# Optimization experiments

Hardware: AMD Instinct MI355X
Metric: run time of the kernel (lower is better)

Reference implementation:

```python
import jax, jax.numpy as jnp
import numpy as np

B = 1024
IN_SIZ = 16384
OUT_SIZ = 16384
C = 8          # channel_siz
NLVL = 10
IFS = IN_SIZ // 2 ** NLVL                                   # 16, in_filter_siz
KLVL = min(int(np.floor(np.log2(OUT_SIZ / 2))), NLVL)       # 10
OFS = OUT_SIZ // 2 ** KLVL                                  # 16, out_filter_siz
STD = 0.9


def setup_inputs() -> dict:
    key = jax.random.key(0)
    ks = jax.random.split(key, 2 * NLVL + 3)
    inp = {}
    inp["x"] = jax.random.normal(ks[0], (B, IN_SIZ, 1), jnp.float32)
    inp["in_filter"] = jax.random.normal(ks[1], (IFS, 1, C), jnp.float32) * STD
    inp["in_bias"] = jnp.zeros((C,), jnp.float32)
    for lvl in range(1, NLVL + 1):
        k = 2 ** lvl
        inp[f"W{lvl}"] = jax.random.normal(ks[2 * lvl], (k, 2, C, C), jnp.float32) * STD
        inp[f"b{lvl}"] = jnp.zeros((k, C), jnp.float32)
    inp["fea_dense"] = jax.random.normal(ks[-1], (2 ** KLVL, C, OFS), jnp.float32) * STD
    return inp


def _level(v, W, b):
    # v: [Kp, B, L, C] parent branches; W: [2*Kp, 2, C, C]; b: [2*Kp, C]
    # kernel-2 stride-2 conv1d: out[t] = relu(x[2t] @ W[0] + x[2t+1] @ W[1] + b)
    Kp, Bn, L, Cc = v.shape
    xp = v.reshape(Kp, Bn, L // 2, 2, Cc)
    xr = jnp.repeat(xp, 2, axis=0)  # child itk reads parent itk // 2
    y = jnp.einsum('kbtsc,kscd->kbtd', xr, W) + b[:, None, None, :]
    return jax.nn.relu(y)


def reference(x, in_filter, in_bias,
              W1, b1, W2, b2, W3, b3, W4, b4, W5, b5,
              W6, b6, W7, b7, W8, b8, W9, b9, W10, b10,
              fea_dense):
    Ws = [W1, W2, W3, W4, W5, W6, W7, W8, W9, W10]
    bs = [b1, b2, b3, b4, b5, b6, b7, b8, b9, b10]
    Bn = x.shape[0]
    # input conv1d: kernel=IFS, stride=IFS (non-overlapping) == blocked matmul
    xin = x[..., 0].reshape(Bn, 2 ** NLVL, IFS)                       # [B, 1024, 16]
    v = jax.nn.relu(jnp.einsum('bnf,fc->bnc', xin, in_filter[:, 0, :]) + in_bias)
    v = v[None]                                                        # [1, B, 1024, C]
    for lvl in range(NLVL):  # klvl == nlvl: all levels branch (tree doubling)
        v = _level(v, Ws[lvl], bs[lvl])
    # v: [2^klvl, B, 1, C] -> per-branch dense feature map
    out = jnp.einsum('kbc,kcf->bkf', v[:, :, 0, :], fea_dense)         # [B, 1024, OFS]
    return out.reshape(Bn, OUT_SIZ, 1)
```

## Files before the change

### kernel.cpp

```cpp
#include <hip/hip_runtime.h>

struct PrepPtrs { const float* W[7]; const float* Bv[7]; const float* F; const float* fb; };

__device__ __forceinline__ int scr(int ci) { return ci ^ ((ci >> 4) & 7); }
__device__ __forceinline__ int cz(int c) { return c ^ ((c >> 3) & 3); }

__device__ __forceinline__ float4 relu4(float4 a) {
  return make_float4(fmaxf(a.x,0.f), fmaxf(a.y,0.f), fmaxf(a.z,0.f), fmaxf(a.w,0.f));
}
__device__ __forceinline__ void fma4(float4& acc, float s, const float4& wv) {
  acc.x = fmaf(s, wv.x, acc.x); acc.y = fmaf(s, wv.y, acc.y);
  acc.z = fmaf(s, wv.z, acc.z); acc.w = fmaf(s, wv.w, acc.w);
}

__global__ void bfly_prep(PrepPtrs P, float* __restrict__ wt) {
  int e = blockIdx.x * 256 + threadIdx.x;
  if (e >= 510 * 68) return;
  int ent = e / 68, r = e % 68, dd = r & 3;
  float v; int dst;
  if (ent < 62) {
    dst = ent * 80 + r;
    if (ent < 60) {
      int lvl, base;
      if (ent < 4)       { lvl = 1; base = 0;  }
      else if (ent < 12) { lvl = 2; base = 4;  }
      else if (ent < 28) { lvl = 3; base = 12; }
      else               { lvl = 4; base = 28; }
      int k = (ent - base) >> 1, th = ent & 1;
      if (r < 64) { int s = r >> 5, c = (r >> 2) & 7;
        v = P.W[lvl-1][k*128 + s*64 + c*8 + th*4 + dd]; }
      else v = P.Bv[lvl-1][k*8 + th*4 + dd];
    } else {
      int th = ent - 60;
      if (r < 64) { int f = r >> 2; v = P.F[f*8 + th*4 + dd]; }
      else v = P.fb[th*4 + dd];
    }
  } else {
    int eb = ent - 62;
    int q = eb / 56, rem = eb % 56;
    int lvl, Kl, base;
    if (rem < 8)       { lvl = 5; Kl = 4;  base = 0;  }
    else if (rem < 24) { lvl = 6; Kl = 8;  base = 8;  }
    else               { lvl = 7; Kl = 16; base = 24; }
    int rr = rem - base, lk = rr >> 1, th = rr & 1;
    int kg = q * Kl + lk;
    if (r < 64) { int s = r >> 5, c = (r >> 2) & 7;
      v = P.W[lvl-1][kg*128 + s*64 + c*8 + th*4 + dd]; }
    else v = P.Bv[lvl-1][kg*8 + th*4 + dd];
    dst = 4960 + eb * 80 + r;
  }
  wt[dst] = v;
}

template<int L>
__device__ __forceinline__ void ka_level(const float4* __restrict__ src,
                                         float4* __restrict__ dst,
                                         const float4* __restrict__ wt4,
                                         int lane, int wq, int th) {
  constexpr int Kc = 1 << L, Tc = 1024 >> L;
  constexpr int entBase = (Kc - 2) * 2;
  constexpr int kIters = (L <= 2) ? 1 : (1 << (L - 2));
  constexpr int tIters = 4 / kIters;
#pragma unroll
  for (int ik = 0; ik < kIters; ++ik) {
    int k;
    if constexpr (L == 1) k = wq & 1;
    else if constexpr (L == 2) k = wq;
    else k = wq + 4 * ik;
    const float4* e4 = wt4 + (entBase + k * 2 + th) * 20;
    const int kp = k >> 1;
#pragma unroll
    for (int it = 0; it < tIters; ++it) {
      int t;
      if constexpr (L == 1) t = lane + (wq >> 1) * 64 + it * 128;
      else if constexpr (L == 2) t = lane + it * 64;
      else if constexpr (L == 3) t = lane + it * 64;
      else t = lane;
      int pb = kp * (2 * Tc) + 2 * t;
      float4 A0 = src[cz(pb)],        C0 = src[cz(pb + 1)];
      float4 A1 = src[cz(pb + 1024)], C1 = src[cz(pb + 1025)];
      float4 a = e4[16];
      fma4(a, A0.x, e4[0]);  fma4(a, A0.y, e4[1]);  fma4(a, A0.z, e4[2]);  fma4(a, A0.w, e4[3]);
      fma4(a, A1.x, e4[4]);  fma4(a, A1.y, e4[5]);  fma4(a, A1.z, e4[6]);  fma4(a, A1.w, e4[7]);
      fma4(a, C0.x, e4[8]);  fma4(a, C0.y, e4[9]);  fma4(a, C0.z, e4[10]); fma4(a, C0.w, e4[11]);
      fma4(a, C1.x, e4[12]); fma4(a, C1.y, e4[13]); fma4(a, C1.z, e4[14]); fma4(a, C1.w, e4[15]);
      dst[cz(th * 1024 + k * Tc + t)] = relu4(a);
    }
  }
}

__global__ __launch_bounds__(512, 2) void bfly_ka(
    const float* __restrict__ x, const float* __restrict__ wt,
    float* __restrict__ st1)
{
  __shared__ float4 sA[2048], sB[2048];
  const int tid = threadIdx.x, b = blockIdx.x;
  const int lane = tid & 63;
  const int wv = __builtin_amdgcn_readfirstlane(tid >> 6);
  const int th = wv & 1, wq = wv >> 1;
  const float4* wt4 = (const float4*)wt;

  {
    const float4* e4 = wt4 + (60 + th) * 20;
    const float* xb = x + (size_t)b * 16384;
#pragma unroll
    for (int i = 0; i < 4; ++i) {
      int n = lane + wq * 64 + i * 256;
      const float4* xr = (const float4*)(xb + n * 16);
      float4 x0 = xr[0], x1 = xr[1], x2 = xr[2], x3 = xr[3];
      float4 a = e4[16];
      fma4(a, x0.x, e4[0]);  fma4(a, x0.y, e4[1]);  fma4(a, x0.z, e4[2]);  fma4(a, x0.w, e4[3]);
      fma4(a, x1.x, e4[4]);  fma4(a, x1.y, e4[5]);  fma4(a, x1.z, e4[6]);  fma4(a, x1.w, e4[7]);
      fma4(a, x2.x, e4[8]);  fma4(a, x2.y, e4[9]);  fma4(a, x2.z, e4[10]); fma4(a, x2.w, e4[11]);
      fma4(a, x3.x, e4[12]); fma4(a, x3.y, e4[13]); fma4(a, x3.z, e4[14]); fma4(a, x3.w, e4[15]);
      sA[cz(th * 1024 + n)] = relu4(a);
    }
  }
  __syncthreads();
  ka_level<1>(sA, sB, wt4, lane, wq, th); __syncthreads();
  ka_level<2>(sB, sA, wt4, lane, wq, th); __syncthreads();
  ka_level<3>(sA, sB, wt4, lane, wq, th); __syncthreads();
  ka_level<4>(sB, sA, wt4, lane, wq, th); __syncthreads();

  float4* o4 = (float4*)st1;
#pragma unroll
  for (int it = 0; it < 4; ++it) {
    int o = tid + it * 512;
    int t4 = o & 63, k4 = (o >> 6) & 15, h = o >> 10;
    o4[((size_t)(h * 16 + k4) * 1024 + b) * 64 + t4] = sA[cz(o)];
  }
}

template<int LV>
__device__ __forceinline__ void kb_level(const float4* __restrict__ src,
                                         float4* __restrict__ dst,
                                         const float4* __restrict__ wb4,
                                         int lane, int wv) {
  constexpr int Kc = 1 << (LV - 3);
  constexpr int Tc = 128 / Kc;
  constexpr int Tp = 256 / Kc;
  constexpr int entB = (LV == 5) ? 0 : (LV == 6) ? 8 : 24;
  constexpr int kIters = Kc / 4;
  constexpr int nIt = 4 / kIters;
  const int th = wv & 1, w2 = wv >> 1;
#pragma unroll
  for (int ik = 0; ik < kIters; ++ik) {
    const int lk = w2 + 4 * ik;
    const float4* e4 = wb4 + (entB + lk * 2 + th) * 20;
    const int lkp = lk >> 1;
#pragma unroll
    for (int it = 0; it < nIt; ++it) {
      int t, bb;
      if constexpr (LV == 5)      { t = lane & 31; bb = (lane >> 5) + it * 2; }
      else if constexpr (LV == 6) { t = lane & 15; bb = (lane >> 4) + it * 4; }
      else                        { t = lane & 7;  bb = lane >> 3; }
      int pb = bb * 256 + lkp * Tp + 2 * t;
      float4 A0 = src[cz(pb)],       C0 = src[cz(pb + 1)];
      float4 A1 = src[cz(pb + 128)], C1 = src[cz(pb + 129)];
      float4 a = e4[16];
      fma4(a, A0.x, e4[0]);  fma4(a, A0.y, e4[1]);  fma4(a, A0.z, e4[2]);  fma4(a, A0.w, e4[3]);
      fma4(a, A1.x, e4[4]);  fma4(a, A1.y, e4[5]);  fma4(a, A1.z, e4[6]);  fma4(a, A1.w, e4[7]);
      fma4(a, C0.x, e4[8]);  fma4(a, C0.y, e4[9]);  fma4(a, C0.z, e4[10]); fma4(a, C0.w, e4[11]);
      fma4(a, C1.x, e4[12]); fma4(a, C1.y, e4[13]); fma4(a, C1.z, e4[14]); fma4(a, C1.w, e4[15]);
      dst[cz(bb * 256 + th * 128 + lk * Tc + t)] = relu4(a);
    }
  }
}

__global__ __launch_bounds__(512, 2) void bfly_kb(
    const float* __restrict__ st1, const float* __restrict__ wt,
    float* __restrict__ st2)
{
  __shared__ float4 s0[2048], s1[2048];
  const int tid = threadIdx.x;
  const int q = blockIdx.x, bt = blockIdx.y;
  const int lane = tid & 63;
  const int wv = __builtin_amdgcn_readfirstlane(tid >> 6);
  const float4* wb4 = (const float4*)wt + 1240 + q * 56 * 20;
  const float4* i4 = (const float4*)st1;

#pragma unroll
  for (int it = 0; it < 4; ++it) {
    int o = tid + it * 512;
    int t4 = o & 63, lk4 = (o >> 6) & 1, h = (o >> 7) & 1, bl = o >> 8;
    float4 v = i4[((size_t)(h * 16 + 2 * q + lk4) * 1024 + bt * 8 + bl) * 64 + t4];
    s0[cz(bl * 256 + h * 128 + lk4 * 64 + t4)] = v;
  }
  __syncthreads();
  kb_level<5>(s0, s1, wb4, lane, wv); __syncthreads();
  kb_level<6>(s1, s0, wb4, lane, wv); __syncthreads();
  kb_level<7>(s0, s1, wb4, lane, wv); __syncthreads();

  float4* o4 = (float4*)st2;
#pragma unroll
  for (int it = 0; it < 4; ++it) {
    int o = tid + it * 512;
    int h = o & 1, t7 = (o >> 1) & 7, bl = (o >> 4) & 7, lk7 = o >> 7;
    float4 v = s1[cz(bl * 256 + h * 128 + lk7 * 8 + t7)];
    o4[(((size_t)(16 * q + lk7) * 1024 + bt * 8 + bl) * 8 + t7) * 2 + h] = v;
  }
}

__global__ __launch_bounds__(256, 4) void bfly_kc(
    const float* __restrict__ st,
    const float* __restrict__ W8, const float* __restrict__ B8,
    const float* __restrict__ W9, const float* __restrict__ B9,
    const float* __restrict__ W10, const float* __restrict__ B10,
    const float* __restrict__ fea, float* __restrict__ out)
{
  __shared__ float4 sA[512], sB[512];
  __shared__ float swt[2928];
  const int tid = threadIdx.x;
  const int j = blockIdx.x, b0 = blockIdx.y * 32;
  const int th = tid & 1, g = tid >> 1;

  {
    const float4* s4 = (const float4*)(st + (size_t)j*65536 + (size_t)b0*64);
#pragma unroll
    for (int it = 0; it < 2; ++it) {
      int idx = tid + it*256;
      sA[scr(idx)] = s4[idx];
    }
  }
  {
    float4* d = (float4*)swt;
    for (int i = tid; i < 64;  i += 256) d[i]       = ((const float4*)(W8  + j*256 ))[i];
    for (int i = tid; i < 128; i += 256) d[64+i]    = ((const float4*)(W9  + j*512 ))[i];
    for (int i = tid; i < 256; i += 256) d[192+i]   = ((const float4*)(W10 + j*1024))[i];
    if (tid < 4)  d[448+tid] = ((const float4*)(B8  + j*16))[tid];
    if (tid < 8)  d[452+tid] = ((const float4*)(B9  + j*32))[tid];
    if (tid < 16) d[460+tid] = ((const float4*)(B10 + j*64))[tid];
    for (int i = tid; i < 256; i += 256) d[476+i]   = ((const float4*)(fea + j*1024))[i];
  }
  __syncthreads();

  auto loadW = [&](int woff, int boff, int k_l, float4* w4, float4& bias) {
#pragma unroll
    for (int s = 0; s < 2; ++s)
#pragma unroll
      for (int c = 0; c < 8; ++c)
        w4[s*8+c] = *(const float4*)(swt + woff + k_l*128 + s*64 + c*8 + th*4);
    bias = *(const float4*)(swt + boff + k_l*8 + th*4);
  };
  auto doItem = [&](const float4* S, float4* D, const float4* w4, float4 bias,
                    int k_l, int bl, int t, int KL, int KPL) {
    int p0 = 2*t*KPL + (k_l >> 1), p1 = p0 + KPL;
    int base = bl * 16;
    float4 A0 = S[scr(base + 2*p0)], A1 = S[scr(base + 2*p0 + 1)];
    float4 C0 = S[scr(base + 2*p1)], C1 = S[scr(base + 2*p1 + 1)];
    float4 a = bias;
    fma4(a, A0.x, w4[0]);  fma4(a, A0.y, w4[1]);  fma4(a, A0.z, w4[2]);  fma4(a, A0.w, w4[3]);
    fma4(a, A1.x, w4[4]);  fma4(a, A1.y, w4[5]);  fma4(a, A1.z, w4[6]);  fma4(a, A1.w, w4[7]);
    fma4(a, C0.x, w4[8]);  fma4(a, C0.y, w4[9]);  fma4(a, C0.z, w4[10]); fma4(a, C0.w, w4[11]);
    fma4(a, C1.x, w4[12]); fma4(a, C1.y, w4[13]); fma4(a, C1.z, w4[14]); fma4(a, C1.w, w4[15]);
    int r = t*KL + k_l;
    D[scr(base + 2*r + th)] = relu4(a);
  };

  { int k_l = g & 1, bl = (g >> 1) & 31, t0 = (g >> 6) * 2;
    float4 w4[16], bias; loadW(0, 1792, k_l, w4, bias);
#pragma unroll
    for (int it = 0; it < 2; ++it) doItem(sA, sB, w4, bias, k_l, bl, t0 + it, 2, 1);
  }
  __syncthreads();
  { int k_l = g & 3, bl = g >> 2;
    float4 w4[16], bias; loadW(256, 1808, k_l, w4, bias);
#pragma unroll
    for (int it = 0; it < 2; ++it) doItem(sB, sA, w4, bias, k_l, bl, it, 4, 2);
  }
  __syncthreads();
  { int k_l = g & 7, bo = g >> 3;
    float4 w4[16], bias; loadW(768, 1840, k_l, w4, bias);
#pragma unroll
    for (int it = 0; it < 2; ++it) doItem(sA, sB, w4, bias, k_l, bo + it*16, 0, 8, 4);
  }
  __syncthreads();
  { int ch = tid & 7, b_l = tid >> 3;
    float* op = out + ((size_t)(b0 + b_l)) * 16384 + j * 128;
#pragma unroll
    for (int it = 0; it < 4; ++it) {
      int cc = ch + it*8, k = cc >> 2, fq = cc & 3;
      float4 s0v = sB[scr(b_l*16 + k*2)];
      float4 s1v = sB[scr(b_l*16 + k*2 + 1)];
      float sc[8] = {s0v.x,s0v.y,s0v.z,s0v.w,s1v.x,s1v.y,s1v.z,s1v.w};
      float4 acc = make_float4(0.f, 0.f, 0.f, 0.f);
#pragma unroll
      for (int c = 0; c < 8; ++c) {
        float4 fv = *(const float4*)(swt + 1904 + k*128 + c*16 + fq*4);
        acc.x = fmaf(sc[c], fv.x, acc.x); acc.y = fmaf(sc[c], fv.y, acc.y);
        acc.z = fmaf(sc[c], fv.z, acc.z); acc.w = fmaf(sc[c], fv.w, acc.w);
      }
      *(float4*)(op + k*16 + fq*4) = acc;
    }
  }
}

extern "C" void kernel_launch(void* const* d_in, const int* in_sizes, int n_in,
                              void* d_out, int out_size, void* d_ws, size_t ws_size,
                              hipStream_t stream) {
  const float* x  = (const float*)d_in[0];
  PrepPtrs P;
  P.F  = (const float*)d_in[1];
  P.fb = (const float*)d_in[2];
  for (int l = 0; l < 7; ++l) {
    P.W[l]  = (const float*)d_in[3 + 2 * l];
    P.Bv[l] = (const float*)d_in[4 + 2 * l];
  }
  const float* W8  = (const float*)d_in[17];
  const float* B8  = (const float*)d_in[18];
  const float* W9  = (const float*)d_in[19];
  const float* B9  = (const float*)d_in[20];
  const float* W10 = (const float*)d_in[21];
  const float* B10 = (const float*)d_in[22];
  const float* fea = (const float*)d_in[23];
  float* wt  = (float*)d_ws;
  float* st2 = (float*)d_ws + 65536;
  float* st1 = (float*)d_out;
  float* out = (float*)d_out;

  bfly_prep<<<dim3(136), dim3(256), 0, stream>>>(P, wt);
  bfly_ka<<<dim3(1024), dim3(512), 0, stream>>>(x, wt, st1);
  bfly_kb<<<dim3(8, 128), dim3(512), 0, stream>>>(st1, wt, st2);
  bfly_kc<<<dim3(128, 32), dim3(256), 0, stream>>>(st2, W8, B8, W9, B9, W10, B10, fea, out);
}
```

Measured before the change: 114.3 us.

## Transpose intermediate staging layout to batch-innermost and remap final-kernel threads

The middle kernel now writes its output with the batch index innermost, and the last kernel reads it with batch-contiguous coalesced loads. The last kernel's shared-memory layout becomes [half][position][batch], so the XOR swizzle is no longer needed. Work is reassigned so each lane handles one batch element and the wave shares the same weights, which should cut shared-memory bank conflicts and address arithmetic. The trade-off is that the middle kernel's global stores now stride across batch, which may scatter its writes.

```diff
diff --git a/kernel.cpp b/kernel.cpp
--- a/kernel.cpp
+++ b/kernel.cpp
@@ -2,7 +2,6 @@
 
 struct PrepPtrs { const float* W[7]; const float* Bv[7]; const float* F; const float* fb; };
 
-__device__ __forceinline__ int scr(int ci) { return ci ^ ((ci >> 4) & 7); }
 __device__ __forceinline__ int cz(int c) { return c ^ ((c >> 3) & 3); }
 
 __device__ __forceinline__ float4 relu4(float4 a) {
@@ -195,9 +194,9 @@
 #pragma unroll
   for (int it = 0; it < 4; ++it) {
     int o = tid + it * 512;
-    int h = o & 1, t7 = (o >> 1) & 7, bl = (o >> 4) & 7, lk7 = o >> 7;
+    int bl = o & 7, t7 = (o >> 3) & 7, h = (o >> 6) & 1, lk7 = o >> 7;
     float4 v = s1[cz(bl * 256 + h * 128 + lk7 * 8 + t7)];
-    o4[(((size_t)(16 * q + lk7) * 1024 + bt * 8 + bl) * 8 + t7) * 2 + h] = v;
+    o4[((size_t)((16 * q + lk7) * 8 + t7) * 2 + h) * 1024 + bt * 8 + bl] = v;
   }
 }
 
@@ -212,14 +211,15 @@
   __shared__ float swt[2928];
   const int tid = threadIdx.x;
   const int j = blockIdx.x, b0 = blockIdx.y * 32;
-  const int th = tid & 1, g = tid >> 1;
-
-  {
-    const float4* s4 = (const float4*)(st + (size_t)j*65536 + (size_t)b0*64);
+  const int bb = tid & 31, grp = tid >> 5;
+
+  {
+    const float4* s4 = (const float4*)st;
 #pragma unroll
     for (int it = 0; it < 2; ++it) {
-      int idx = tid + it*256;
-      sA[scr(idx)] = s4[idx];
+      int idx = tid + it * 256;
+      int t = idx >> 6, h = (idx >> 5) & 1, bl = idx & 31;
+      sA[h * 256 + t * 32 + bl] = s4[((size_t)((j * 8 + t) * 2 + h)) * 1024 + b0 + bl];
     }
   }
   {
@@ -234,7 +234,7 @@
   }
   __syncthreads();
 
-  auto loadW = [&](int woff, int boff, int k_l, float4* w4, float4& bias) {
+  auto loadW = [&](int woff, int boff, int k_l, int th, float4* w4, float4& bias) {
 #pragma unroll
     for (int s = 0; s < 2; ++s)
 #pragma unroll
@@ -242,46 +242,60 @@
         w4[s*8+c] = *(const float4*)(swt + woff + k_l*128 + s*64 + c*8 + th*4);
     bias = *(const float4*)(swt + boff + k_l*8 + th*4);
   };
-  auto doItem = [&](const float4* S, float4* D, const float4* w4, float4 bias,
-                    int k_l, int bl, int t, int KL, int KPL) {
-    int p0 = 2*t*KPL + (k_l >> 1), p1 = p0 + KPL;
-    int base = bl * 16;
-    float4 A0 = S[scr(base + 2*p0)], A1 = S[scr(base + 2*p0 + 1)];
-    float4 C0 = S[scr(base + 2*p1)], C1 = S[scr(base + 2*p1 + 1)];
+  auto mat = [&](const float4& A0, const float4& A1, const float4& C0, const float4& C1,
+                 const float4* w4, float4 bias) {
     float4 a = bias;
     fma4(a, A0.x, w4[0]);  fma4(a, A0.y, w4[1]);  fma4(a, A0.z, w4[2]);  fma4(a, A0.w, w4[3]);
     fma4(a, A1.x, w4[4]);  fma4(a, A1.y, w4[5]);  fma4(a, A1.z, w4[6]);  fma4(a, A1.w, w4[7]);
     fma4(a, C0.x, w4[8]);  fma4(a, C0.y, w4[9]);  fma4(a, C0.z, w4[10]); fma4(a, C0.w, w4[11]);
     fma4(a, C1.x, w4[12]); fma4(a, C1.y, w4[13]); fma4(a, C1.z, w4[14]); fma4(a, C1.w, w4[15]);
-    int r = t*KL + k_l;
-    D[scr(base + 2*r + th)] = relu4(a);
+    return relu4(a);
   };
 
-  { int k_l = g & 1, bl = (g >> 1) & 31, t0 = (g >> 6) * 2;
-    float4 w4[16], bias; loadW(0, 1792, k_l, w4, bias);
-#pragma unroll
-    for (int it = 0; it < 2; ++it) doItem(sA, sB, w4, bias, k_l, bl, t0 + it, 2, 1);
-  }
-  __syncthreads();
-  { int k_l = g & 3, bl = g >> 2;
-    float4 w4[16], bias; loadW(256, 1808, k_l, w4, bias);
-#pragma unroll
-    for (int it = 0; it < 2; ++it) doItem(sB, sA, w4, bias, k_l, bl, it, 4, 2);
-  }
-  __syncthreads();
-  { int k_l = g & 7, bo = g >> 3;
-    float4 w4[16], bias; loadW(768, 1840, k_l, w4, bias);
-#pragma unroll
-    for (int it = 0; it < 2; ++it) doItem(sA, sB, w4, bias, k_l, bo + it*16, 0, 8, 4);
-  }
-  __syncthreads();
-  { int ch = tid & 7, b_l = tid >> 3;
+  {
+    int h = grp >> 2, k = (grp >> 1) & 1, ti = grp & 1;
+    float4 w4[16], bias; loadW(0, 1792, k, h, w4, bias);
+#pragma unroll
+    for (int i = 0; i < 2; ++i) {
+      int t = ti + 2 * i;
+      float4 A0 = sA[(2*t) * 32 + bb],     A1 = sA[256 + (2*t) * 32 + bb];
+      float4 C0 = sA[(2*t+1) * 32 + bb],   C1 = sA[256 + (2*t+1) * 32 + bb];
+      sB[h * 256 + (2*t + k) * 32 + bb] = mat(A0, A1, C0, C1, w4, bias);
+    }
+  }
+  __syncthreads();
+  {
+    int h = grp >> 2, k9 = grp & 3;
+    float4 w4[16], bias; loadW(256, 1808, k9, h, w4, bias);
+#pragma unroll
+    for (int t9 = 0; t9 < 2; ++t9) {
+      int p0 = 4 * t9 + (k9 >> 1), p1 = p0 + 2;
+      float4 A0 = sB[p0 * 32 + bb], A1 = sB[256 + p0 * 32 + bb];
+      float4 C0 = sB[p1 * 32 + bb], C1 = sB[256 + p1 * 32 + bb];
+      sA[h * 256 + (t9 * 4 + k9) * 32 + bb] = mat(A0, A1, C0, C1, w4, bias);
+    }
+  }
+  __syncthreads();
+  {
+    int k10 = grp;
+    int p0 = k10 >> 1, p1 = p0 + 4;
+    float4 A0 = sA[p0 * 32 + bb], A1 = sA[256 + p0 * 32 + bb];
+    float4 C0 = sA[p1 * 32 + bb], C1 = sA[256 + p1 * 32 + bb];
+#pragma unroll
+    for (int h = 0; h < 2; ++h) {
+      float4 w4[16], bias; loadW(768, 1840, k10, h, w4, bias);
+      sB[h * 256 + k10 * 32 + bb] = mat(A0, A1, C0, C1, w4, bias);
+    }
+  }
+  __syncthreads();
+  {
+    int ch = tid & 7, b_l = tid >> 3;
     float* op = out + ((size_t)(b0 + b_l)) * 16384 + j * 128;
 #pragma unroll
     for (int it = 0; it < 4; ++it) {
       int cc = ch + it*8, k = cc >> 2, fq = cc & 3;
-      float4 s0v = sB[scr(b_l*16 + k*2)];
-      float4 s1v = sB[scr(b_l*16 + k*2 + 1)];
+      float4 s0v = sB[k * 32 + b_l];
+      float4 s1v = sB[256 + k * 32 + b_l];
       float sc[8] = {s0v.x,s0v.y,s0v.z,s0v.w,s1v.x,s1v.y,s1v.z,s1v.w};
       float4 acc = make_float4(0.f, 0.f, 0.f, 0.f);
 #pragma unroll
```

Measured after the change: 97.07 us. -15.1%, faster.
